# Kernel tuning notes

Measured on AMD Instinct MI355X. Metric: run time of the kernel, lower is better.

Reference implementation:

```python
import jax, jax.numpy as jnp
import numpy as np
from jax import lax

EPS = 1e-5  # BatchNorm eps; eval-mode BN with running_mean=0, running_var=1


def _bn(v, g, b):
    return v * (g / jnp.sqrt(1.0 + EPS)) + b


def setup_inputs() -> dict:
    key = jax.random.key(0)
    ks = jax.random.split(key, 8)
    B, I, O, H, W, E, K, r = 16, 128, 128, 128, 128, 16, 3, 8
    Ir, Or = I // r, O // r
    f = jax.random.normal
    return {
        "x": f(ks[0], (B, I, H, W), jnp.float32),
        "experts": f(ks[1], (E, O, I, K, K), jnp.float32) * 0.05,
        "rw1": f(ks[2], (Ir, I), jnp.float32) * 0.05,
        "rbn1_g": jnp.ones((Ir,), jnp.float32),
        "rbn1_b": jnp.zeros((Ir,), jnp.float32),
        "rw2": f(ks[3], (I, Ir), jnp.float32) * 0.05,
        "rbn2_g": jnp.ones((I,), jnp.float32),
        "rbn2_b": jnp.zeros((I,), jnp.float32),
        "rw3": f(ks[4], (E, I), jnp.float32) * 0.05,
        "rb3": jnp.zeros((E,), jnp.float32),
        "ca_w1": f(ks[5], (Or, O), jnp.float32) * 0.05,
        "ca_bn1_g": jnp.ones((Or,), jnp.float32),
        "ca_bn1_b": jnp.zeros((Or,), jnp.float32),
        "ca_w2": f(ks[6], (O, Or), jnp.float32) * 0.05,
        "ca_bn2_g": jnp.ones((O,), jnp.float32),
        "ca_bn2_b": jnp.zeros((O,), jnp.float32),
        "sa_w": f(ks[7], (1, 2, 7, 7), jnp.float32) * 0.05,
        "sa_bn_g": jnp.ones((1,), jnp.float32),
        "sa_bn_b": jnp.zeros((1,), jnp.float32),
    }


def reference(x, experts, rw1, rbn1_g, rbn1_b, rw2, rbn2_g, rbn2_b, rw3, rb3,
              ca_w1, ca_bn1_g, ca_bn1_b, ca_w2, ca_bn2_g, ca_bn2_b,
              sa_w, sa_bn_g, sa_bn_b):
    B, I, H, W = x.shape
    E, O, _, K, _ = experts.shape
    # --- routing: avgpool -> 1x1 conv (matmul) -> BN -> ReLU -> 1x1 -> BN -> sigmoid -> 1x1 -> softmax
    p = jnp.mean(x, axis=(2, 3))                                  # [B, I]
    h = jax.nn.relu(_bn(p @ rw1.T, rbn1_g, rbn1_b))               # [B, I/r]
    g = jax.nn.sigmoid(_bn(h @ rw2.T, rbn2_g, rbn2_b))            # [B, I]
    rweights = jax.nn.softmax(g @ rw3.T + rb3, axis=1)            # [B, E]
    # --- expert-weighted kernel generation as a single GEMM
    w = jnp.einsum('be,eoihw->boihw', rweights, experts)          # [B, O, I, K, K]
    # --- per-sample conv via grouped conv (groups = B), stride=1, padding=1
    out = lax.conv_general_dilated(
        x.reshape(1, B * I, H, W),
        w.reshape(B * O, I, K, K),
        window_strides=(1, 1), padding=((1, 1), (1, 1)),
        dimension_numbers=('NCHW', 'OIHW', 'NCHW'),
        feature_group_count=B,
    ).reshape(B, O, H, W)
    # --- SE channel attention
    cp = jnp.mean(out, axis=(2, 3))                               # [B, O]
    ch = jax.nn.relu(_bn(cp @ ca_w1.T, ca_bn1_g, ca_bn1_b))
    cw = jax.nn.sigmoid(_bn(ch @ ca_w2.T, ca_bn2_g, ca_bn2_b))    # [B, O]
    out = out * cw[:, :, None, None]
    # --- CBAM spatial attention
    sp = jnp.concatenate([jnp.mean(out, axis=1, keepdims=True),
                          jnp.max(out, axis=1, keepdims=True)], axis=1)  # [B,2,H,W]
    sw = lax.conv_general_dilated(sp, sa_w, (1, 1), ((3, 3), (3, 3)),
                                  dimension_numbers=('NCHW', 'OIHW', 'NCHW'))
    sw = jax.nn.sigmoid(_bn(sw, sa_bn_g.reshape(1, 1, 1, 1), sa_bn_b.reshape(1, 1, 1, 1)))
    out = out * sw
    # --- residual (in_channels == out_channels -> Identity)
    return out + x
```

## Files before the change

### kernel.cpp

```cpp
#include <hip/hip_runtime.h>

typedef unsigned short ushort_t;
typedef __attribute__((ext_vector_type(4))) float float4_t;
typedef __attribute__((ext_vector_type(8))) short short8_t;
typedef __attribute__((ext_vector_type(8))) unsigned short ushort8_t;

__device__ __forceinline__ ushort_t f2bf(float f) {
    unsigned u = __builtin_bit_cast(unsigned, f);
    u = (u + 0x7fffu + ((u >> 16) & 1u)) >> 16;
    return (ushort_t)u;
}

__device__ __forceinline__ void gld16(const void* g, void* l) {
    __builtin_amdgcn_global_load_lds(
        (const __attribute__((address_space(1))) unsigned int*)g,
        (__attribute__((address_space(3))) unsigned int*)l, 16, 0, 0);
}


__global__ __launch_bounds__(256) void init_kernel(float* __restrict__ p, float* __restrict__ cp,
                                                   float* __restrict__ sp, ushort_t* __restrict__ xn) {
    int t = blockIdx.x * 256 + threadIdx.x;
    if (t < 2048) { p[t] = 0.f; return; }
    if (t < 4096) { cp[t - 2048] = 0.f; return; }
    if (t < 4096 + 574592) { sp[t - 4096] = 0.f; return; }
    int e = t - (4096 + 574592);
    if (e < 1056768) {
        int b = e / 66048;
        int r = e % 66048;
        int pix = r >> 7, i = r & 127;
        int hp, wp;
        if (pix < 130)      { hp = 0;   wp = pix; }
        else if (pix < 260) { hp = 129; wp = pix - 130; }
        else { int q = pix - 260; hp = 1 + (q >> 1); wp = (q & 1) ? 129 : 0; }
        xn[((b * 130 + hp) * 130 + wp) * 128 + i] = 0;
    }
}

__global__ __launch_bounds__(256) void transpose_kernel(const float* __restrict__ x,
                                                        ushort_t* __restrict__ xn,
                                                        float* __restrict__ p) {
    __shared__ float tile[128][65];
    int blk = blockIdx.x;
    int wt = blk & 1, h = (blk >> 1) & 127, b = blk >> 8;
    int w0 = wt * 64;
    int tid = threadIdx.x;
    int wl = tid & 63, ig = tid >> 6;
    const float* src = x + ((long)(b * 128) * 128 + h) * 128 + w0 + wl;
    #pragma unroll
    for (int i = ig; i < 128; i += 4) tile[i][wl] = src[(long)i * 16384];
    __syncthreads();
    if (tid < 128) {
        float s = 0.f;
        #pragma unroll
        for (int w = 0; w < 64; ++w) s += tile[tid][w];
        atomicAdd(&p[b * 128 + tid], s * (1.0f / 16384.0f));
    }
    int l16 = tid & 15, wq = tid >> 4;
    #pragma unroll
    for (int pass = 0; pass < 4; ++pass) {
        int w = wq + pass * 16;
        ushort8_t v;
        #pragma unroll
        for (int j = 0; j < 8; ++j) v[j] = f2bf(tile[l16 * 8 + j][w]);
        *(ushort8_t*)&xn[((b * 130 + h + 1) * 130 + (w0 + w + 1)) * 128 + l16 * 8] = v;
    }
}

__global__ __launch_bounds__(256) void routing_kernel(const float* __restrict__ p,
        const float* __restrict__ rw1, const float* __restrict__ g1, const float* __restrict__ b1,
        const float* __restrict__ rw2, const float* __restrict__ g2, const float* __restrict__ b2,
        const float* __restrict__ rw3, const float* __restrict__ rb3, float* __restrict__ rwt) {
    __shared__ float sh[16][16];
    __shared__ float sg[16][128];
    __shared__ float sl[16][16];
    int tid = threadIdx.x;
    const float bns = rsqrtf(1.0f + 1e-5f);
    {   int b = tid >> 4, j = tid & 15;
        float s = 0.f;
        for (int i = 0; i < 128; ++i) s += p[b * 128 + i] * rw1[j * 128 + i];
        s = s * (g1[j] * bns) + b1[j];
        sh[b][j] = fmaxf(s, 0.f); }
    __syncthreads();
    for (int c = 0; c < 8; ++c) {
        int idx = tid + c * 256;
        int b = idx >> 7, j = idx & 127;
        float s = 0.f;
        for (int k = 0; k < 16; ++k) s += sh[b][k] * rw2[j * 16 + k];
        s = s * (g2[j] * bns) + b2[j];
        sg[b][j] = 1.0f / (1.0f + expf(-s));
    }
    __syncthreads();
    {   int b = tid >> 4, e = tid & 15;
        float s = rb3[e];
        for (int j = 0; j < 128; ++j) s += sg[b][j] * rw3[e * 128 + j];
        sl[b][e] = s; }
    __syncthreads();
    {   int b = tid >> 4, e = tid & 15;
        float m = -1e30f;
        for (int k = 0; k < 16; ++k) m = fmaxf(m, sl[b][k]);
        float num = expf(sl[b][e] - m), den = 0.f;
        for (int k = 0; k < 16; ++k) den += expf(sl[b][k] - m);
        rwt[b * 16 + e] = num / den; }
}

__global__ __launch_bounds__(256) void wgen_kernel(const float* __restrict__ experts,
                                                   const float* __restrict__ rwt,
                                                   ushort_t* __restrict__ w2) {
    int b = blockIdx.x >> 7, o = blockIdx.x & 127;
    int tid = threadIdx.x;
    int i = tid & 127, eh = tid >> 7;
    __shared__ float rw[16];
    __shared__ float part[9][128];
    if (tid < 16) rw[tid] = rwt[b * 16 + tid];
    __syncthreads();
    float acc[9] = {0, 0, 0, 0, 0, 0, 0, 0, 0};
    const float* ep = experts + (long)(eh * 8) * 147456 + (o * 128 + i) * 9;
    #pragma unroll
    for (int e = 0; e < 8; ++e) {
        float r = rw[eh * 8 + e];
        const float* q = ep + (long)e * 147456;
        #pragma unroll
        for (int d = 0; d < 9; ++d) acc[d] += r * q[d];
    }
    if (eh) {
        #pragma unroll
        for (int d = 0; d < 9; ++d) part[d][i] = acc[d];
    }
    __syncthreads();
    if (!eh) {
        #pragma unroll
        for (int d = 0; d < 9; ++d)
            w2[((b * 9 + d) << 14) + (o << 7) + i] = f2bf(acc[d] + part[d][i]);
    }
}

struct __align__(16) ConvSmem {
    union {
        struct { ushort_t X[16640]; ushort_t A[4][4096]; } t;
        float c[4224];
    };
};

__global__ __launch_bounds__(256, 2) void conv_kernel(const ushort_t* __restrict__ xn,
                                                      const ushort_t* __restrict__ w2,
                                                      float* __restrict__ out,
                                                      float* __restrict__ cp) {
    __shared__ ConvSmem sm;
    int bh = (blockIdx.x & 7) * 256 + (blockIdx.x >> 3);
    int b = bh >> 7, h = bh & 127;
    int tid = threadIdx.x;
    int lane = tid & 63, wave = tid >> 6;
    int wm = wave & 1, wn = wave >> 1;
    int q = lane >> 4, nl = lane & 15;

    float4_t acc[4][4];
    #pragma unroll
    for (int mi = 0; mi < 4; ++mi)
        #pragma unroll
        for (int ni = 0; ni < 4; ++ni) acc[mi][ni] = (float4_t){0.f, 0.f, 0.f, 0.f};

    const ushort_t* xbase = xn + (b * 130 + h) * 16640;
    const ushort_t* abase = w2 + (long)b * 147456;

    auto stageX = [&](int dy) {
        const ushort_t* xrow = xbase + dy * 16640;
        #pragma unroll
        for (int seg = wave; seg < 33; seg += 4) {
            if (seg < 32 || lane < 32) {
                int lofs = seg * 512 + lane * 8;
                int pp = lofs >> 7;
                int jb = (lofs & 127) >> 3;
                gld16(xrow + (pp << 7) + ((jb ^ (pp & 15)) << 3), &sm.t.X[seg * 512]);
            }
        }
    };
    auto stageA = [&](int c) {
        int dy = c / 12, rem = c % 12, dx = rem >> 2, ic = rem & 3;
        const ushort_t* ab = abase + (dy * 3 + dx) * 16384 + ic * 32;
        int buf = c & 3;
        int ol = lane >> 2;
        int jsrc = (lane & 3) ^ ((ol >> 1) & 3);
        #pragma unroll
        for (int inst = 0; inst < 2; ++inst) {
            int ob = wave * 32 + inst * 16;
            gld16(ab + (ob + ol) * 128 + (jsrc << 3), &sm.t.A[buf][ob * 32]);
        }
    };

    short8_t afr[2][4], bfr[2][4];
    auto readFrag = [&](int cc) {
        int pb = cc & 1;
        int dx = (cc % 12) >> 2, ic = cc & 3;
        const ushort_t* ap = &sm.t.A[cc & 3][0];
        #pragma unroll
        for (int mi = 0; mi < 4; ++mi) {
            int o = wm * 64 + mi * 16 + nl;
            afr[pb][mi] = *(const short8_t*)&ap[(o << 5) + ((q ^ ((o >> 1) & 3)) << 3)];
        }
        #pragma unroll
        for (int ni = 0; ni < 4; ++ni) {
            int pp = wn * 64 + ni * 16 + nl + dx;
            int J = ic * 4 + q;
            bfr[pb][ni] = *(const short8_t*)&sm.t.X[(pp << 7) + ((J ^ (pp & 15)) << 3)];
        }
    };
    auto domfma = [&](int pb) {
        __builtin_amdgcn_s_setprio(1);
        #pragma unroll
        for (int mi = 0; mi < 4; ++mi)
            #pragma unroll
            for (int ni = 0; ni < 4; ++ni)
                acc[mi][ni] = __builtin_amdgcn_mfma_f32_16x16x32_bf16(
                    afr[pb][mi], bfr[pb][ni], acc[pb ? mi : mi][ni], 0, 0, 0);
        __builtin_amdgcn_s_setprio(0);
    };

    stageX(0);
    stageA(0); stageA(1); stageA(2);
    asm volatile("s_waitcnt vmcnt(0)" ::: "memory");
    __builtin_amdgcn_s_barrier();
    readFrag(0);

    #pragma unroll
    for (int c = 0; c < 36; ++c) {
        if (c + 3 < 36) stageA(c + 3);
        const bool bnd = (c == 11 || c == 23);
        if (!bnd && c + 1 < 36) readFrag(c + 1);
        domfma(c & 1);
        if (bnd) {
            __builtin_amdgcn_s_barrier();
            stageX(c == 11 ? 1 : 2);
            asm volatile("s_waitcnt vmcnt(0)" ::: "memory");
            __builtin_amdgcn_s_barrier();
            readFrag(c + 1);
        } else if (c < 35) {
            if (c == 33)
                asm volatile("s_waitcnt vmcnt(0)" ::: "memory");
            else if (!(c == 0 || c == 12 || c == 24 || c == 34))
                asm volatile("s_waitcnt vmcnt(2)" ::: "memory");
            __builtin_amdgcn_s_barrier();
        }
    }

    #pragma unroll
    for (int mi = 0; mi < 4; ++mi) {
        int o0 = wm * 64 + mi * 16 + q * 4;
        float rs[4] = {0.f, 0.f, 0.f, 0.f};
        #pragma unroll
        for (int ni = 0; ni < 4; ++ni) {
            float4_t v = acc[mi][ni];
            #pragma unroll
            for (int r = 0; r < 4; ++r) rs[r] += v[r];
        }
        #pragma unroll
        for (int r = 0; r < 4; ++r) {
            for (int msk = 1; msk < 16; msk <<= 1) rs[r] += __shfl_xor(rs[r], msk, 64);
            if (nl == 0) atomicAdd(&cp[(b << 7) + o0 + r], rs[r]);
        }
    }

    float* outb = out + (((long)(b << 7)) << 14) + (h << 7);
    #pragma unroll
    for (int os = 0; os < 4; ++os) {
        __syncthreads();
        if (wm == (os >> 1)) {
            #pragma unroll
            for (int mi2 = 0; mi2 < 2; ++mi2) {
                int mi = (os & 1) * 2 + mi2;
                #pragma unroll
                for (int ni = 0; ni < 4; ++ni) {
                    float4_t v = acc[mi][ni];
                    int orow = mi2 * 16 + q * 4;
                    int w = wn * 64 + ni * 16 + nl;
                    #pragma unroll
                    for (int rr = 0; rr < 4; ++rr) sm.c[(orow + rr) * 132 + w] = v[rr];
                }
            }
        }
        __syncthreads();
        int row = tid >> 3, j8 = tid & 7;
        float* og = outb + ((long)(os * 32 + row) << 14);
        #pragma unroll
        for (int k = 0; k < 4; ++k) {
            float4_t v = *(const float4_t*)&sm.c[row * 132 + j8 * 4 + k * 32];
            *(float4_t*)&og[j8 * 4 + k * 32] = v;
        }
    }
}

__global__ __launch_bounds__(256) void se_kernel(const float* __restrict__ cp,
        const float* __restrict__ w1, const float* __restrict__ g1, const float* __restrict__ b1,
        const float* __restrict__ w2, const float* __restrict__ g2, const float* __restrict__ b2,
        float* __restrict__ cw) {
    __shared__ float sc[16][128];
    __shared__ float sh[16][16];
    int tid = threadIdx.x;
    const float bns = rsqrtf(1.0f + 1e-5f);
    for (int c = 0; c < 8; ++c) {
        int idx = tid + c * 256;
        sc[idx >> 7][idx & 127] = cp[idx] * (1.0f / 16384.0f);
    }
    __syncthreads();
    {   int b = tid >> 4, j = tid & 15;
        float s = 0.f;
        for (int o = 0; o < 128; ++o) s += sc[b][o] * w1[j * 128 + o];
        s = s * (g1[j] * bns) + b1[j];
        sh[b][j] = fmaxf(s, 0.f); }
    __syncthreads();
    for (int c = 0; c < 8; ++c) {
        int idx = tid + c * 256;
        int b = idx >> 7, o = idx & 127;
        float s = 0.f;
        for (int k = 0; k < 16; ++k) s += sh[b][k] * w2[o * 16 + k];
        s = s * (g2[o] * bns) + b2[o];
        cw[idx] = 1.0f / (1.0f + expf(-s));
    }
}

__global__ __launch_bounds__(256) void stat_kernel(const float* __restrict__ out,
                                                   const float* __restrict__ cw,
                                                   float* __restrict__ sp) {
    int b = blockIdx.x >> 7, h = blockIdx.x & 127;
    int tid = threadIdx.x;
    int w = tid & 127, oh = tid >> 7;
    __shared__ float scw[128], ssum[128], smax[128];
    if (tid < 128) scw[tid] = cw[(b << 7) + tid];
    __syncthreads();
    const float* src = out + ((long)b << 21) + ((long)(oh * 64) << 14) + (h << 7) + w;
    float s = 0.f, m = -1e30f;
    #pragma unroll 8
    for (int o = 0; o < 64; ++o) {
        float v = src[(long)o << 14] * scw[oh * 64 + o];
        s += v;
        m = fmaxf(m, v);
    }
    if (oh) { ssum[w] = s; smax[w] = m; }
    __syncthreads();
    if (!oh) {
        s += ssum[w];
        m = fmaxf(m, smax[w]);
        float* d = sp + b * 2 * 17956;
        d[(h + 3) * 134 + (w + 3)] = s * (1.0f / 128.0f);
        d[17956 + (h + 3) * 134 + (w + 3)] = m;
    }
}

__global__ __launch_bounds__(256) void sattn_kernel(const float* __restrict__ sp,
        const float* __restrict__ k98, const float* __restrict__ g, const float* __restrict__ bb,
        const float* __restrict__ cw, const float* __restrict__ x, float* __restrict__ out) {
    int b = blockIdx.x >> 7, h = blockIdx.x & 127;
    int tid = threadIdx.x;
    __shared__ float ls[2][7][134];
    __shared__ float lk[98];
    __shared__ float sws[128];
    __shared__ float scw[128];
    const float* sb = sp + b * 2 * 17956;
    for (int idx = tid; idx < 2 * 7 * 134; idx += 256) {
        int c = idx / 938, rr = idx % 938;
        int ky = rr / 134, wp = rr % 134;
        ls[c][ky][wp] = sb[c * 17956 + (h + ky) * 134 + wp];
    }
    if (tid < 98) lk[tid] = k98[tid];
    if (tid >= 128) scw[tid - 128] = cw[(b << 7) + (tid - 128)];
    __syncthreads();
    if (tid < 128) {
        float s = 0.f;
        #pragma unroll
        for (int c = 0; c < 2; ++c)
            #pragma unroll
            for (int ky = 0; ky < 7; ++ky)
                #pragma unroll
                for (int kx = 0; kx < 7; ++kx)
                    s += ls[c][ky][tid + kx] * lk[c * 49 + ky * 7 + kx];
        s = s * (g[0] * rsqrtf(1.0f + 1e-5f)) + bb[0];
        sws[tid] = 1.0f / (1.0f + expf(-s));
    }
    __syncthreads();
    int w4 = tid & 31, og = tid >> 5;
    long base = (((long)b << 21) + (h << 7)) + (w4 << 2);
    float4_t sv = *(const float4_t*)&sws[w4 << 2];
    #pragma unroll
    for (int o = og; o < 128; o += 8) {
        long idx = base + ((long)o << 14);
        float4_t ov = *(const float4_t*)&out[idx];
        float4_t xv = *(const float4_t*)&x[idx];
        float4_t r = ov * scw[o] * sv + xv;
        *(float4_t*)&out[idx] = r;
    }
}

extern "C" void kernel_launch(void* const* d_in, const int* in_sizes, int n_in,
                              void* d_out, int out_size, void* d_ws, size_t ws_size,
                              hipStream_t stream) {
    const float* x       = (const float*)d_in[0];
    const float* experts = (const float*)d_in[1];
    const float* rw1     = (const float*)d_in[2];
    const float* rbn1_g  = (const float*)d_in[3];
    const float* rbn1_b  = (const float*)d_in[4];
    const float* rw2     = (const float*)d_in[5];
    const float* rbn2_g  = (const float*)d_in[6];
    const float* rbn2_b  = (const float*)d_in[7];
    const float* rw3     = (const float*)d_in[8];
    const float* rb3     = (const float*)d_in[9];
    const float* ca_w1   = (const float*)d_in[10];
    const float* ca_bn1g = (const float*)d_in[11];
    const float* ca_bn1b = (const float*)d_in[12];
    const float* ca_w2   = (const float*)d_in[13];
    const float* ca_bn2g = (const float*)d_in[14];
    const float* ca_bn2b = (const float*)d_in[15];
    const float* sa_w    = (const float*)d_in[16];
    const float* sa_g    = (const float*)d_in[17];
    const float* sa_b    = (const float*)d_in[18];
    float* out = (float*)d_out;
    char* ws = (char*)d_ws;

    ushort_t* xn  = (ushort_t*)(ws);
    ushort_t* w2  = (ushort_t*)(ws + 69222400);
    float*    p   = (float*)(ws + 73940992);
    float*    cp  = (float*)(ws + 73949184);
    float*    rwt = (float*)(ws + 73957376);
    float*    cw  = (float*)(ws + 73958400);
    float*    sp  = (float*)(ws + 73966592);

    hipLaunchKernelGGL(init_kernel, dim3(6389), dim3(256), 0, stream, p, cp, sp, xn);
    hipLaunchKernelGGL(transpose_kernel, dim3(4096), dim3(256), 0, stream, x, xn, p);
    hipLaunchKernelGGL(routing_kernel, dim3(1), dim3(256), 0, stream,
                       p, rw1, rbn1_g, rbn1_b, rw2, rbn2_g, rbn2_b, rw3, rb3, rwt);
    hipLaunchKernelGGL(wgen_kernel, dim3(2048), dim3(256), 0, stream, experts, rwt, w2);
    hipLaunchKernelGGL(conv_kernel, dim3(2048), dim3(256), 0, stream, xn, w2, out, cp);
    hipLaunchKernelGGL(se_kernel, dim3(1), dim3(256), 0, stream,
                       cp, ca_w1, ca_bn1g, ca_bn1b, ca_w2, ca_bn2g, ca_bn2b, cw);
    hipLaunchKernelGGL(stat_kernel, dim3(2048), dim3(256), 0, stream, out, cw, sp);
    hipLaunchKernelGGL(sattn_kernel, dim3(2048), dim3(256), 0, stream,
                       sp, sa_w, sa_g, sa_b, cw, x, out);
}
```

Baseline: 489.8 us.

## Fuse routing into weight generation and SE MLP into stat kernel

The single-block routing kernel is folded into the weight-generation kernel. Each of 128 blocks, one per output channel, recomputes the routing softmax for all 16 samples while asynchronously loading that channel's expert slice into LDS. It then produces the mixed weights for all batches from that slice, so experts are read once instead of once per batch. The single-block SE MLP is likewise folded into stat_kernel: each block recomputes its sample's channel weights, and row 0 writes cw for the later kernel. This removes two serial one-block launches and redundant expert traffic, at the cost of redundant small MLP work per block, a large LDS footprint, and only 128 blocks for weight generation.

```diff
diff --git a/kernel.cpp b/kernel.cpp
--- a/kernel.cpp
+++ b/kernel.cpp
@@ -67,14 +67,34 @@
     }
 }
 
-__global__ __launch_bounds__(256) void routing_kernel(const float* __restrict__ p,
+__global__ __launch_bounds__(256) void wgen_kernel(const float* __restrict__ experts,
+        const float* __restrict__ p,
         const float* __restrict__ rw1, const float* __restrict__ g1, const float* __restrict__ b1,
         const float* __restrict__ rw2, const float* __restrict__ g2, const float* __restrict__ b2,
-        const float* __restrict__ rw3, const float* __restrict__ rb3, float* __restrict__ rwt) {
+        const float* __restrict__ rw3, const float* __restrict__ rb3,
+        ushort_t* __restrict__ w2) {
+    int o = blockIdx.x;
+    int tid = threadIdx.x;
+    int lane = tid & 63, wave = tid >> 6;
+    __shared__ __align__(16) float ex[16 * 1152];
+    __shared__ float sg[16][128];
     __shared__ float sh[16][16];
-    __shared__ float sg[16][128];
     __shared__ float sl[16][16];
-    int tid = threadIdx.x;
+    __shared__ float rwl[16][16];
+
+    const float* ebase = experts + (long)o * 1152;
+    #pragma unroll
+    for (int j = 0; j < 4; ++j) {
+        int e = wave * 4 + j;
+        const char* src = (const char*)(ebase + (long)e * 147456) + lane * 16;
+        char* dst = (char*)&ex[e * 1152];
+        #pragma unroll
+        for (int k = 0; k < 5; ++k) {
+            if (k < 4 || lane < 32)
+                gld16(src + k * 1024, dst + k * 1024);
+        }
+    }
+
     const float bns = rsqrtf(1.0f + 1e-5f);
     {   int b = tid >> 4, j = tid & 15;
         float s = 0.f;
@@ -101,38 +121,32 @@
         for (int k = 0; k < 16; ++k) m = fmaxf(m, sl[b][k]);
         float num = expf(sl[b][e] - m), den = 0.f;
         for (int k = 0; k < 16; ++k) den += expf(sl[b][k] - m);
-        rwt[b * 16 + e] = num / den; }
-}
-
-__global__ __launch_bounds__(256) void wgen_kernel(const float* __restrict__ experts,
-                                                   const float* __restrict__ rwt,
-                                                   ushort_t* __restrict__ w2) {
-    int b = blockIdx.x >> 7, o = blockIdx.x & 127;
-    int tid = threadIdx.x;
-    int i = tid & 127, eh = tid >> 7;
-    __shared__ float rw[16];
-    __shared__ float part[9][128];
-    if (tid < 16) rw[tid] = rwt[b * 16 + tid];
-    __syncthreads();
-    float acc[9] = {0, 0, 0, 0, 0, 0, 0, 0, 0};
-    const float* ep = experts + (long)(eh * 8) * 147456 + (o * 128 + i) * 9;
-    #pragma unroll
-    for (int e = 0; e < 8; ++e) {
-        float r = rw[eh * 8 + e];
-        const float* q = ep + (long)e * 147456;
-        #pragma unroll
-        for (int d = 0; d < 9; ++d) acc[d] += r * q[d];
-    }
-    if (eh) {
-        #pragma unroll
-        for (int d = 0; d < 9; ++d) part[d][i] = acc[d];
-    }
-    __syncthreads();
-    if (!eh) {
+        rwl[b][e] = num / den; }
+    asm volatile("s_waitcnt vmcnt(0)" ::: "memory");
+    __syncthreads();
+
+    int i = tid & 127, half = tid >> 7;
+    float acc[8][9];
+    #pragma unroll
+    for (int b = 0; b < 8; ++b)
+        #pragma unroll
+        for (int d = 0; d < 9; ++d) acc[b][d] = 0.f;
+    for (int e = 0; e < 16; ++e) {
+        float v[9];
+        #pragma unroll
+        for (int d = 0; d < 9; ++d) v[d] = ex[e * 1152 + i * 9 + d];
+        #pragma unroll
+        for (int b = 0; b < 8; ++b) {
+            float r = rwl[half * 8 + b][e];
+            #pragma unroll
+            for (int d = 0; d < 9; ++d) acc[b][d] += v[d] * r;
+        }
+    }
+    #pragma unroll
+    for (int b = 0; b < 8; ++b)
         #pragma unroll
         for (int d = 0; d < 9; ++d)
-            w2[((b * 9 + d) << 14) + (o << 7) + i] = f2bf(acc[d] + part[d][i]);
-    }
+            w2[(((half * 8 + b) * 9 + d) << 14) + (o << 7) + i] = f2bf(acc[b][d]);
 }
 
 struct __align__(16) ConvSmem {
@@ -212,7 +226,7 @@
             #pragma unroll
             for (int ni = 0; ni < 4; ++ni)
                 acc[mi][ni] = __builtin_amdgcn_mfma_f32_16x16x32_bf16(
-                    afr[pb][mi], bfr[pb][ni], acc[pb ? mi : mi][ni], 0, 0, 0);
+                    afr[pb][mi], bfr[pb][ni], acc[mi][ni], 0, 0, 0);
         __builtin_amdgcn_s_setprio(0);
     };
 
@@ -289,44 +303,34 @@
     }
 }
 
-__global__ __launch_bounds__(256) void se_kernel(const float* __restrict__ cp,
+__global__ __launch_bounds__(256) void stat_kernel(const float* __restrict__ out,
+        const float* __restrict__ cp,
         const float* __restrict__ w1, const float* __restrict__ g1, const float* __restrict__ b1,
         const float* __restrict__ w2, const float* __restrict__ g2, const float* __restrict__ b2,
-        float* __restrict__ cw) {
-    __shared__ float sc[16][128];
-    __shared__ float sh[16][16];
-    int tid = threadIdx.x;
-    const float bns = rsqrtf(1.0f + 1e-5f);
-    for (int c = 0; c < 8; ++c) {
-        int idx = tid + c * 256;
-        sc[idx >> 7][idx & 127] = cp[idx] * (1.0f / 16384.0f);
-    }
-    __syncthreads();
-    {   int b = tid >> 4, j = tid & 15;
-        float s = 0.f;
-        for (int o = 0; o < 128; ++o) s += sc[b][o] * w1[j * 128 + o];
-        s = s * (g1[j] * bns) + b1[j];
-        sh[b][j] = fmaxf(s, 0.f); }
-    __syncthreads();
-    for (int c = 0; c < 8; ++c) {
-        int idx = tid + c * 256;
-        int b = idx >> 7, o = idx & 127;
-        float s = 0.f;
-        for (int k = 0; k < 16; ++k) s += sh[b][k] * w2[o * 16 + k];
-        s = s * (g2[o] * bns) + b2[o];
-        cw[idx] = 1.0f / (1.0f + expf(-s));
-    }
-}
-
-__global__ __launch_bounds__(256) void stat_kernel(const float* __restrict__ out,
-                                                   const float* __restrict__ cw,
-                                                   float* __restrict__ sp) {
+        float* __restrict__ cw, float* __restrict__ sp) {
     int b = blockIdx.x >> 7, h = blockIdx.x & 127;
     int tid = threadIdx.x;
+    __shared__ float scp[128], sch[16], scw[128], ssum[128], smax[128];
+    const float bns = rsqrtf(1.0f + 1e-5f);
+    if (tid < 128) scp[tid] = cp[(b << 7) + tid] * (1.0f / 16384.0f);
+    __syncthreads();
+    if (tid < 16) {
+        float s = 0.f;
+        for (int o = 0; o < 128; ++o) s += scp[o] * w1[tid * 128 + o];
+        s = s * (g1[tid] * bns) + b1[tid];
+        sch[tid] = fmaxf(s, 0.f);
+    }
+    __syncthreads();
+    if (tid < 128) {
+        float s = 0.f;
+        #pragma unroll
+        for (int k = 0; k < 16; ++k) s += sch[k] * w2[tid * 16 + k];
+        s = s * (g2[tid] * bns) + b2[tid];
+        scw[tid] = 1.0f / (1.0f + expf(-s));
+        if (h == 0) cw[(b << 7) + tid] = scw[tid];
+    }
+    __syncthreads();
     int w = tid & 127, oh = tid >> 7;
-    __shared__ float scw[128], ssum[128], smax[128];
-    if (tid < 128) scw[tid] = cw[(b << 7) + tid];
-    __syncthreads();
     const float* src = out + ((long)b << 21) + ((long)(oh * 64) << 14) + (h << 7) + w;
     float s = 0.f, m = -1e30f;
     #pragma unroll 8
@@ -419,19 +423,16 @@
     ushort_t* w2  = (ushort_t*)(ws + 69222400);
     float*    p   = (float*)(ws + 73940992);
     float*    cp  = (float*)(ws + 73949184);
-    float*    rwt = (float*)(ws + 73957376);
     float*    cw  = (float*)(ws + 73958400);
     float*    sp  = (float*)(ws + 73966592);
 
     hipLaunchKernelGGL(init_kernel, dim3(6389), dim3(256), 0, stream, p, cp, sp, xn);
     hipLaunchKernelGGL(transpose_kernel, dim3(4096), dim3(256), 0, stream, x, xn, p);
-    hipLaunchKernelGGL(routing_kernel, dim3(1), dim3(256), 0, stream,
-                       p, rw1, rbn1_g, rbn1_b, rw2, rbn2_g, rbn2_b, rw3, rb3, rwt);
-    hipLaunchKernelGGL(wgen_kernel, dim3(2048), dim3(256), 0, stream, experts, rwt, w2);
+    hipLaunchKernelGGL(wgen_kernel, dim3(128), dim3(256), 0, stream,
+                       experts, p, rw1, rbn1_g, rbn1_b, rw2, rbn2_g, rbn2_b, rw3, rb3, w2);
     hipLaunchKernelGGL(conv_kernel, dim3(2048), dim3(256), 0, stream, xn, w2, out, cp);
-    hipLaunchKernelGGL(se_kernel, dim3(1), dim3(256), 0, stream,
-                       cp, ca_w1, ca_bn1g, ca_bn1b, ca_w2, ca_bn2g, ca_bn2b, cw);
-    hipLaunchKernelGGL(stat_kernel, dim3(2048), dim3(256), 0, stream, out, cw, sp);
+    hipLaunchKernelGGL(stat_kernel, dim3(2048), dim3(256), 0, stream,
+                       out, cp, ca_w1, ca_bn1g, ca_bn1b, ca_w2, ca_bn2g, ca_bn2b, cw, sp);
     hipLaunchKernelGGL(sattn_kernel, dim3(2048), dim3(256), 0, stream,
                        sp, sa_w, sa_g, sa_b, cw, x, out);
 }
```

Result: no change. 482.8 us (-1.4%).
